# Performance work log

Hardware: AMD Instinct MI355X
Metric: run time of the kernel (lower is better)

The kernel has to match this reference:

```python
import jax, jax.numpy as jnp
import numpy as np

EMBED_DIM = 1024

def setup_inputs() -> dict:
    key = jax.random.key(0)
    kx, kwq, kbq, kwk, kbk, kwv, kbv = jax.random.split(key, 7)
    d = EMBED_DIM
    s = 1.0 / np.sqrt(d)
    x = jax.random.normal(kx, (4, 2048, d), dtype=jnp.float32)
    # nn.Linear weights are [out, in]; we store transposed [in, out] for x @ W
    Wq = jax.random.uniform(kwq, (d, d), jnp.float32, -s, s)
    bq = jax.random.uniform(kbq, (d,), jnp.float32, -s, s)
    Wk = jax.random.uniform(kwk, (d, d), jnp.float32, -s, s)
    bk = jax.random.uniform(kbk, (d,), jnp.float32, -s, s)
    Wv = jax.random.uniform(kwv, (d, d), jnp.float32, -s, s)
    bv = jax.random.uniform(kbv, (d,), jnp.float32, -s, s)
    return {"x": x, "Wq": Wq, "bq": bq, "Wk": Wk, "bk": bk, "Wv": Wv, "bv": bv}

def reference(x, Wq, bq, Wk, bk, Wv, bv):
    d = x.shape[-1]
    q = x @ Wq + bq            # [B, S, D]
    k = x @ Wk + bk            # [B, S, D]
    v = x @ Wv + bv            # [B, S, D]
    scores = jnp.einsum('bsd,btd->bst', q, k) / jnp.sqrt(jnp.asarray(d, x.dtype))
    attn = jax.nn.softmax(scores, axis=-1)  # [B, S, S]
    return jnp.einsum('bst,btd->bsd', attn, v)
```

## Files before the change

kernel.cpp:

```cpp
#include <hip/hip_runtime.h>
#include <hip/hip_bf16.h>
#include <stdint.h>


typedef short bf16x8 __attribute__((ext_vector_type(8)));
typedef float f32x4 __attribute__((ext_vector_type(4)));
typedef unsigned short us4 __attribute__((ext_vector_type(4)));
typedef unsigned short us;

#define B_ 4
#define S_ 2048
#define D_ 1024

__device__ __forceinline__ us f2bf(float f) {
  unsigned int u = __float_as_uint(f);
  unsigned int r = (u + 0x7fffu + ((u >> 16) & 1u)) >> 16;
  return (us)r;
}

__device__ __forceinline__ void gl2lds16(void* lds, const void* g) {
  __builtin_amdgcn_global_load_lds(
      (const __attribute__((address_space(1))) unsigned int*)(uintptr_t)g,
      (__attribute__((address_space(3))) unsigned int*)(uintptr_t)lds,
      16, 0, 0);
}

__device__ __forceinline__ void sched_fence() { __builtin_amdgcn_sched_barrier(0); }
__device__ __forceinline__ void barrier_f() {
  sched_fence(); __builtin_amdgcn_s_barrier(); sched_fence();
}

template<int BM, int R0, int R1>
__device__ __forceinline__ void stageR(us* buf, const us* gA, size_t sA,
                                       const us* gB, size_t sB,
                                       int wave, int lane) {
  int slot = ((lane & 7) ^ (lane >> 3)) << 4;
  char* l = (char*)buf;
#pragma unroll
  for (int r = R0; r < R1; ++r) {
    int row = r * 64 + wave * 8 + (lane >> 3);
    const char* src;
    if (r * 64 < BM)
      src = (const char*)gA + (size_t)row * sA + slot;
    else
      src = (const char*)gB + (size_t)(row - BM) * sB + slot;
    gl2lds16(l + r * 8192 + wave * 1024, src);
  }
}

template<int EPI, int BM, int BN, int WNS>
__global__ __launch_bounds__(512, 2) void gemm8p(
    const us* __restrict__ Aall, const us* __restrict__ Ball,
    size_t aBatch, size_t bBatch, int sAe, int sBe, int nt,
    const float* __restrict__ bq, const float* __restrict__ bk,
    const float* __restrict__ bv, void* __restrict__ outp,
    us* __restrict__ vtb, const float* __restrict__ rsum) {
  __shared__ __align__(16) us lds[3][(BM + BN) * 64];
  int tid = threadIdx.x, lane = tid & 63, wave = tid >> 6;
  int wm = wave / WNS, wn = wave % WNS;
  int m0 = blockIdx.x * BM, n0 = blockIdx.y * BN;
  size_t bz = blockIdx.z;
  const us* gA = Aall + bz * aBatch + (size_t)m0 * sAe;
  const us* gB = Ball + bz * bBatch + (size_t)n0 * sBe;
  size_t sA = (size_t)sAe * 2, sB = (size_t)sBe * 2;

  stageR<BM, 0, 6>(lds[0], gA, sA, gB, sB, wave, lane);
  stageR<BM, 0, 6>(lds[1], gA + 64, sA, gB + 64, sB, wave, lane);

  int r15 = lane & 15, kg = lane >> 4, l7 = lane & 7;
  int x0 = (kg ^ l7) << 4;
  f32x4 acc[4][4] = {};

  for (int t = 0; t < nt; ++t) {
    if (t == nt - 1) asm volatile("s_waitcnt vmcnt(0)" ::: "memory");
    else             asm volatile("s_waitcnt vmcnt(6)" ::: "memory");
    barrier_f();
    const us* buf = lds[t % 3];
    us* nbuf = (us*)lds[(t + 2) % 3];
    bool dostage = (t + 2 < nt);
    const us* gA2 = gA + (size_t)(t + 2) * 64;
    const us* gB2 = gB + (size_t)(t + 2) * 64;
    const char* pa = (const char*)buf + (size_t)(wm * 64 + r15) * 128;
    const char* pb = (const char*)buf + (size_t)(BM + wn * 64 + r15) * 128;

    if (dostage) stageR<BM, 0, 3>(nbuf, gA2, sA, gB2, sB, wave, lane);
    bf16x8 A0[4], B0[4];
#pragma unroll
    for (int f = 0; f < 4; ++f) A0[f] = *(const bf16x8*)(pa + f * 2048 + x0);
#pragma unroll
    for (int f = 0; f < 4; ++f) B0[f] = *(const bf16x8*)(pb + f * 2048 + x0);
    __builtin_amdgcn_s_setprio(1);
#pragma unroll
    for (int fn = 0; fn < 4; ++fn)
#pragma unroll
      for (int fm = 0; fm < 4; ++fm)
        acc[fm][fn] = __builtin_amdgcn_mfma_f32_16x16x32_bf16(A0[fm], B0[fn], acc[fm][fn], 0, 0, 0);
    __builtin_amdgcn_s_setprio(0);

    if (dostage) stageR<BM, 3, 6>(nbuf, gA2, sA, gB2, sB, wave, lane);
    bf16x8 A1[4], B1[4];
#pragma unroll
    for (int f = 0; f < 4; ++f) A1[f] = *(const bf16x8*)(pa + f * 2048 + (x0 ^ 64));
#pragma unroll
    for (int f = 0; f < 4; ++f) B1[f] = *(const bf16x8*)(pb + f * 2048 + (x0 ^ 64));
    __builtin_amdgcn_s_setprio(1);
#pragma unroll
    for (int fn = 0; fn < 4; ++fn)
#pragma unroll
      for (int fm = 0; fm < 4; ++fm)
        acc[fm][fn] = __builtin_amdgcn_mfma_f32_16x16x32_bf16(A1[fm], B1[fn], acc[fm][fn], 0, 0, 0);
    __builtin_amdgcn_s_setprio(0);
  }

  if constexpr (EPI == 0) {
#pragma unroll
    for (int fm = 0; fm < 4; ++fm)
#pragma unroll
      for (int fn = 0; fn < 4; ++fn) {
        int col = n0 + wn * 64 + fn * 16 + r15;
        int row0 = m0 + wm * 64 + fm * 16 + (kg << 2);
        int mat = col >> 10;
        const float* bp = (mat == 0) ? bq : (mat == 1) ? bk : bv;
        float bb = bp[col & 1023];
        if (mat < 2) {
          us* ob = (us*)outp + ((size_t)mat << 23);
#pragma unroll
          for (int r = 0; r < 4; ++r)
            ob[(size_t)(row0 + r) * D_ + (col & 1023)] = f2bf(acc[fm][fn][r] + bb);
        } else {
          int b = row0 >> 11, trow = row0 & 2047, dcol = col & 1023;
          us4 v4 = {f2bf(acc[fm][fn][0] + bb), f2bf(acc[fm][fn][1] + bb),
                    f2bf(acc[fm][fn][2] + bb), f2bf(acc[fm][fn][3] + bb)};
          *(us4*)(vtb + (size_t)b * D_ * S_ + (size_t)dcol * S_ + trow) = v4;
        }
      }
  } else {
    float* ob = (float*)outp + bz * (size_t)(S_ * D_);
    const float* rs = rsum + bz * (size_t)S_;
#pragma unroll
    for (int fm = 0; fm < 4; ++fm) {
      int row0 = m0 + wm * 64 + fm * 16 + (kg << 2);
      float inv[4];
#pragma unroll
      for (int r = 0; r < 4; ++r) inv[r] = 1.0f / rs[row0 + r];
#pragma unroll
      for (int fn = 0; fn < 4; ++fn) {
        int col = n0 + wn * 64 + fn * 16 + r15;
#pragma unroll
        for (int r = 0; r < 4; ++r)
          ob[(size_t)(row0 + r) * D_ + col] = acc[fm][fn][r] * inv[r];
      }
    }
  }
}

__global__ __launch_bounds__(512, 2) void s2p(
    const us* __restrict__ Aall, const us* __restrict__ Ball,
    us* __restrict__ pball, float* __restrict__ rsum) {
  __shared__ __align__(16) us lds3[3][16384];
  const int tid = threadIdx.x, lane = tid & 63, wave = tid >> 6;
  const int wm = wave >> 2, wn = wave & 3;
  const int m0 = blockIdx.x * 256, n0 = blockIdx.y * 256;
  const size_t bz = blockIdx.z;
  const char* gA = (const char*)(Aall + bz * (size_t)(S_ * D_) + (size_t)m0 * D_);
  const char* gB = (const char*)(Ball + bz * (size_t)(S_ * D_) + (size_t)n0 * D_);
  const size_t sA = (size_t)D_ * 2, sB = (size_t)D_ * 2;
  const int nt = 32;

  const int r15 = lane & 15, kg = lane >> 4;
  const int srcslot = (((lane & 3) ^ ((lane >> 3) & 3)) << 4);
  const int srow = wave * 16 + (lane >> 2);

  auto stage = [&](int bi, int t) {
    char* l = (char*)lds3[bi];
    const size_t koff = (size_t)t * 64;
#pragma unroll
    for (int r = 0; r < 4; ++r) {
      int row = r * 128 + srow;
      const char* src = (row < 256)
          ? gA + (size_t)row * sA + koff + srcslot
          : gB + (size_t)(row - 256) * sB + koff + srcslot;
      gl2lds16(l + r * 8192 + wave * 1024, src);
    }
  };

  stage(0, 0);
  stage(1, 1);

  f32x4 acc[8][4] = {};
  for (int t = 0; t < nt; ++t) {
    if (t == nt - 1) asm volatile("s_waitcnt vmcnt(0)" ::: "memory");
    else             asm volatile("s_waitcnt vmcnt(4)" ::: "memory");
    barrier_f();
    if (t + 2 < nt) stage((t + 2) % 3, t + 2);
    const char* buf = (const char*)lds3[t % 3];

    bf16x8 Af[8], Bf[4];
#pragma unroll
    for (int f = 0; f < 8; ++f) {
      int tr = wm * 128 + f * 16 + r15;
      Af[f] = *(const bf16x8*)(buf + tr * 64 + ((kg ^ ((tr >> 1) & 3)) << 4));
    }
#pragma unroll
    for (int n = 0; n < 4; ++n) {
      int tr = 256 + wn * 64 + n * 16 + r15;
      Bf[n] = *(const bf16x8*)(buf + tr * 64 + ((kg ^ ((tr >> 1) & 3)) << 4));
    }
    __builtin_amdgcn_s_setprio(1);
#pragma unroll
    for (int n = 0; n < 4; ++n)
#pragma unroll
      for (int f = 0; f < 8; ++f)
        acc[f][n] = __builtin_amdgcn_mfma_f32_16x16x32_bf16(Af[f], Bf[n], acc[f][n], 0, 0, 0);
    __builtin_amdgcn_s_setprio(0);
  }

  us* pbase = pball + bz * (size_t)(S_ * S_);
  float* rsb = rsum + bz * (size_t)S_;
#pragma unroll
  for (int fm = 0; fm < 8; ++fm) {
    int row0 = m0 + wm * 128 + fm * 16 + (kg << 2);
    float psum[4] = {0.f, 0.f, 0.f, 0.f};
#pragma unroll
    for (int fn = 0; fn < 4; ++fn) {
      int col = n0 + wn * 64 + fn * 16 + r15;
#pragma unroll
      for (int r = 0; r < 4; ++r) {
        float p = __expf(acc[fm][fn][r] * 0.03125f);
        pbase[(size_t)(row0 + r) * S_ + col] = f2bf(p);
        psum[r] += p;
      }
    }
#pragma unroll
    for (int r = 0; r < 4; ++r) {
      float s = psum[r];
      s += __shfl_xor(s, 1);
      s += __shfl_xor(s, 2);
      s += __shfl_xor(s, 4);
      s += __shfl_xor(s, 8);
      if (r15 == 0) atomicAdd(&rsb[row0 + r], s);
    }
  }
}

__global__ __launch_bounds__(256) void prep_all(
    const float* __restrict__ Wq, const float* __restrict__ Wk,
    const float* __restrict__ Wv, const float* __restrict__ x,
    us* __restrict__ wtb, us* __restrict__ xb, float* __restrict__ rsum) {
  __shared__ us hs[64][65];
  int blk = blockIdx.x, tid = threadIdx.x;
  if (blk < 4096) {
    size_t i = ((size_t)blk * 256 + tid) * 8;
    float4 f0 = *(const float4*)(x + i);
    float4 f1 = *(const float4*)(x + i + 4);
    float vals[8] = {f0.x, f0.y, f0.z, f0.w, f1.x, f1.y, f1.z, f1.w};
    union { bf16x8 v; us s_[8]; } H;
#pragma unroll
    for (int e = 0; e < 8; ++e) H.s_[e] = f2bf(vals[e]);
    *(bf16x8*)(xb + i) = H.v;
  } else if (blk < 4864) {
    int bb = blk - 4096;
    int mat = bb >> 8, n0 = (bb & 15) * 64, k0 = ((bb >> 4) & 15) * 64;
    const float* W = (mat == 0) ? Wq : (mat == 1) ? Wk : Wv;
#pragma unroll
    for (int i = 0; i < 16; ++i) {
      int idx = tid + i * 256;
      int r = idx >> 6, c = idx & 63;
      hs[r][c] = f2bf(W[(size_t)(k0 + r) * D_ + (n0 + c)]);
    }
    __syncthreads();
    us* o = wtb + ((size_t)mat << 20);
#pragma unroll
    for (int i = 0; i < 16; ++i) {
      int idx = tid + i * 256;
      int r = idx >> 6, c = idx & 63;
      o[(size_t)(n0 + r) * D_ + (k0 + c)] = hs[c][r];
    }
  } else {
    int idx = (blk - 4864) * 256 + tid;
    ((float4*)rsum)[idx] = (float4){0.f, 0.f, 0.f, 0.f};
  }
}

extern "C" void kernel_launch(void* const* d_in, const int* in_sizes, int n_in,
                              void* d_out, int out_size, void* d_ws, size_t ws_size,
                              hipStream_t stream) {
  const float* x  = (const float*)d_in[0];
  const float* Wq = (const float*)d_in[1];
  const float* bq = (const float*)d_in[2];
  const float* Wk = (const float*)d_in[3];
  const float* bk = (const float*)d_in[4];
  const float* Wv = (const float*)d_in[5];
  const float* bv = (const float*)d_in[6];
  float* out = (float*)d_out;
  char* ws = (char*)d_ws;
  const size_t MB = 1024 * 1024;
  us* qb   = (us*)(ws + 0 * MB);
  us* kb   = (us*)(ws + 16 * MB);
  us* vtb  = (us*)(ws + 32 * MB);
  us* wtb  = (us*)(ws + 48 * MB);
  us* xb   = (us*)(ws + 54 * MB);
  us* pb   = (us*)(ws + 70 * MB);
  float* rsum = (float*)(ws + 102 * MB);

  prep_all<<<dim3(4872), 256, 0, stream>>>(Wq, Wk, Wv, x, wtb, xb, rsum);
  gemm8p<0, 128, 256, 4><<<dim3(64, 12, 1), 512, 0, stream>>>(
      xb, wtb, 0, 0, D_, D_, 16, bq, bk, bv, qb, vtb, nullptr);
  s2p<<<dim3(8, 8, 4), 512, 0, stream>>>(qb, kb, pb, rsum);
  gemm8p<2, 256, 128, 2><<<dim3(8, 8, 4), 512, 0, stream>>>(
      pb, vtb, (size_t)S_ * S_, (size_t)D_ * S_, S_, S_, 32,
      nullptr, nullptr, nullptr, out, nullptr, rsum);
}
```

Baseline: 143.7 us.

## Split QKV projection into 256x256-tile Q/K GEMM and separate V GEMM

The fused QKV projection is split in two. Q and K are now produced by the larger 256x256-tile score GEMM kernel, which gains a bias+bf16 epilogue through a template parameter. V keeps the 128x256 kernel and its transposed-store epilogue, writing V^T directly. The aim is more data reuse per tile for the Q/K half, at the cost of an extra kernel launch, and the Q/K grid of 256 blocks may fill the GPU less evenly.

```diff
diff --git a/kernel.cpp b/kernel.cpp
--- a/kernel.cpp
+++ b/kernel.cpp
@@ -52,7 +52,6 @@
 __global__ __launch_bounds__(512, 2) void gemm8p(
     const us* __restrict__ Aall, const us* __restrict__ Ball,
     size_t aBatch, size_t bBatch, int sAe, int sBe, int nt,
-    const float* __restrict__ bq, const float* __restrict__ bk,
     const float* __restrict__ bv, void* __restrict__ outp,
     us* __restrict__ vtb, const float* __restrict__ rsum) {
   __shared__ __align__(16) us lds[3][(BM + BN) * 64];
@@ -112,27 +111,18 @@
     __builtin_amdgcn_s_setprio(0);
   }
 
-  if constexpr (EPI == 0) {
+  if constexpr (EPI == 4) {
 #pragma unroll
     for (int fm = 0; fm < 4; ++fm)
 #pragma unroll
       for (int fn = 0; fn < 4; ++fn) {
         int col = n0 + wn * 64 + fn * 16 + r15;
         int row0 = m0 + wm * 64 + fm * 16 + (kg << 2);
-        int mat = col >> 10;
-        const float* bp = (mat == 0) ? bq : (mat == 1) ? bk : bv;
-        float bb = bp[col & 1023];
-        if (mat < 2) {
-          us* ob = (us*)outp + ((size_t)mat << 23);
-#pragma unroll
-          for (int r = 0; r < 4; ++r)
-            ob[(size_t)(row0 + r) * D_ + (col & 1023)] = f2bf(acc[fm][fn][r] + bb);
-        } else {
-          int b = row0 >> 11, trow = row0 & 2047, dcol = col & 1023;
-          us4 v4 = {f2bf(acc[fm][fn][0] + bb), f2bf(acc[fm][fn][1] + bb),
-                    f2bf(acc[fm][fn][2] + bb), f2bf(acc[fm][fn][3] + bb)};
-          *(us4*)(vtb + (size_t)b * D_ * S_ + (size_t)dcol * S_ + trow) = v4;
-        }
+        float bb = bv[col];
+        int b = row0 >> 11, trow = row0 & 2047;
+        us4 v4 = {f2bf(acc[fm][fn][0] + bb), f2bf(acc[fm][fn][1] + bb),
+                  f2bf(acc[fm][fn][2] + bb), f2bf(acc[fm][fn][3] + bb)};
+        *(us4*)(vtb + (size_t)b * D_ * S_ + (size_t)col * S_ + trow) = v4;
       }
   } else {
     float* ob = (float*)outp + bz * (size_t)(S_ * D_);
@@ -154,16 +144,19 @@
   }
 }
 
-__global__ __launch_bounds__(512, 2) void s2p(
+template<int EPI>
+__global__ __launch_bounds__(512, 2) void gemmS(
     const us* __restrict__ Aall, const us* __restrict__ Ball,
-    us* __restrict__ pball, float* __restrict__ rsum) {
+    size_t aBatch, size_t bBatch,
+    const float* __restrict__ bq, const float* __restrict__ bk,
+    us* __restrict__ outb, float* __restrict__ rsum) {
   __shared__ __align__(16) us lds3[3][16384];
   const int tid = threadIdx.x, lane = tid & 63, wave = tid >> 6;
   const int wm = wave >> 2, wn = wave & 3;
   const int m0 = blockIdx.x * 256, n0 = blockIdx.y * 256;
   const size_t bz = blockIdx.z;
-  const char* gA = (const char*)(Aall + bz * (size_t)(S_ * D_) + (size_t)m0 * D_);
-  const char* gB = (const char*)(Ball + bz * (size_t)(S_ * D_) + (size_t)n0 * D_);
+  const char* gA = (const char*)(Aall + bz * aBatch + (size_t)m0 * D_);
+  const char* gB = (const char*)(Ball + bz * bBatch + (size_t)n0 * D_);
   const size_t sA = (size_t)D_ * 2, sB = (size_t)D_ * 2;
   const int nt = 32;
 
@@ -215,30 +208,46 @@
     __builtin_amdgcn_s_setprio(0);
   }
 
-  us* pbase = pball + bz * (size_t)(S_ * S_);
-  float* rsb = rsum + bz * (size_t)S_;
-#pragma unroll
-  for (int fm = 0; fm < 8; ++fm) {
-    int row0 = m0 + wm * 128 + fm * 16 + (kg << 2);
-    float psum[4] = {0.f, 0.f, 0.f, 0.f};
-#pragma unroll
-    for (int fn = 0; fn < 4; ++fn) {
-      int col = n0 + wn * 64 + fn * 16 + r15;
+  if constexpr (EPI == 0) {
+#pragma unroll
+    for (int fm = 0; fm < 8; ++fm)
+#pragma unroll
+      for (int fn = 0; fn < 4; ++fn) {
+        int col = n0 + wn * 64 + fn * 16 + r15;
+        int row0 = m0 + wm * 128 + fm * 16 + (kg << 2);
+        int mat = col >> 10;
+        float bb = (mat ? bk : bq)[col & 1023];
+        us* ob = outb + ((size_t)mat << 23);
+#pragma unroll
+        for (int r = 0; r < 4; ++r)
+          ob[(size_t)(row0 + r) * D_ + (col & 1023)] = f2bf(acc[fm][fn][r] + bb);
+      }
+  } else {
+    us* pbase = outb + bz * (size_t)(S_ * S_);
+    float* rsb = rsum + bz * (size_t)S_;
+#pragma unroll
+    for (int fm = 0; fm < 8; ++fm) {
+      int row0 = m0 + wm * 128 + fm * 16 + (kg << 2);
+      float psum[4] = {0.f, 0.f, 0.f, 0.f};
+#pragma unroll
+      for (int fn = 0; fn < 4; ++fn) {
+        int col = n0 + wn * 64 + fn * 16 + r15;
+#pragma unroll
+        for (int r = 0; r < 4; ++r) {
+          float p = __expf(acc[fm][fn][r] * 0.03125f);
+          pbase[(size_t)(row0 + r) * S_ + col] = f2bf(p);
+          psum[r] += p;
+        }
+      }
 #pragma unroll
       for (int r = 0; r < 4; ++r) {
-        float p = __expf(acc[fm][fn][r] * 0.03125f);
-        pbase[(size_t)(row0 + r) * S_ + col] = f2bf(p);
-        psum[r] += p;
-      }
-    }
-#pragma unroll
-    for (int r = 0; r < 4; ++r) {
-      float s = psum[r];
-      s += __shfl_xor(s, 1);
-      s += __shfl_xor(s, 2);
-      s += __shfl_xor(s, 4);
-      s += __shfl_xor(s, 8);
-      if (r15 == 0) atomicAdd(&rsb[row0 + r], s);
+        float s = psum[r];
+        s += __shfl_xor(s, 1);
+        s += __shfl_xor(s, 2);
+        s += __shfl_xor(s, 4);
+        s += __shfl_xor(s, 8);
+        if (r15 == 0) atomicAdd(&rsb[row0 + r], s);
+      }
     }
   }
 }
@@ -302,12 +311,16 @@
   us* xb   = (us*)(ws + 54 * MB);
   us* pb   = (us*)(ws + 70 * MB);
   float* rsum = (float*)(ws + 102 * MB);
+  (void)kb;
 
   prep_all<<<dim3(4872), 256, 0, stream>>>(Wq, Wk, Wv, x, wtb, xb, rsum);
-  gemm8p<0, 128, 256, 4><<<dim3(64, 12, 1), 512, 0, stream>>>(
-      xb, wtb, 0, 0, D_, D_, 16, bq, bk, bv, qb, vtb, nullptr);
-  s2p<<<dim3(8, 8, 4), 512, 0, stream>>>(qb, kb, pb, rsum);
+  gemmS<0><<<dim3(32, 8, 1), 512, 0, stream>>>(
+      xb, wtb, 0, 0, bq, bk, qb, nullptr);
+  gemm8p<4, 128, 256, 4><<<dim3(64, 4, 1), 512, 0, stream>>>(
+      xb, wtb + ((size_t)2 << 20), 0, 0, D_, D_, 16, bv, nullptr, vtb, nullptr);
+  gemmS<1><<<dim3(8, 8, 4), 512, 0, stream>>>(
+      qb, kb, (size_t)S_ * D_, (size_t)S_ * D_, nullptr, nullptr, pb, rsum);
   gemm8p<2, 256, 128, 2><<<dim3(8, 8, 4), 512, 0, stream>>>(
       pb, vtb, (size_t)S_ * S_, (size_t)D_ * S_, S_, S_, 32,
-      nullptr, nullptr, nullptr, out, nullptr, rsum);
-}
+      nullptr, out, nullptr, rsum);
+}
```

New measurement: 142.0 us, median of 3. About the same (-1.2%).
